# Performance work log

Hardware: AMD Instinct MI355X
Metric: run time of the kernel (lower is better)

The kernel has to match this reference:

```python
import jax, jax.numpy as jnp
import numpy as np

B, IN_SEQ, HID_SEQ, OUT_SEQ = 2, 2048, 2048, 2048
C_IN, C_OUT, H = 1024, 1024, 16
HD = C_OUT // H  # 64


def _linear_params(key, out_f, in_f):
    kw, kb = jax.random.split(key)
    bound = 1.0 / np.sqrt(in_f)
    w = jax.random.uniform(kw, (out_f, in_f), jnp.float32, -bound, bound)
    b = jax.random.uniform(kb, (out_f,), jnp.float32, -bound, bound)
    return w, b


def setup_inputs() -> dict:
    key = jax.random.key(0)
    ks = jax.random.split(key, 6)
    x = jax.random.normal(ks[0], (B, IN_SEQ, C_IN), jnp.float32)
    w_hseq, b_hseq = _linear_params(ks[1], HID_SEQ, IN_SEQ)
    wq, bq = _linear_params(ks[2], C_OUT, C_IN)
    wk, bk = _linear_params(ks[3], C_OUT, C_IN)
    wv, bv = _linear_params(ks[4], C_OUT, C_IN)
    w_oseq, b_oseq = _linear_params(ks[5], OUT_SEQ, HID_SEQ)
    return {"x": x, "w_hseq": w_hseq, "b_hseq": b_hseq,
            "wq": wq, "bq": bq, "wk": wk, "bk": bk, "wv": wv, "bv": bv,
            "w_oseq": w_oseq, "b_oseq": b_oseq}


def reference(x, w_hseq, b_hseq, wq, bq, wk, bk, wv, bv, w_oseq, b_oseq):
    b = x.shape[0]
    # seq-axis projection: Linear(in_seq -> hidden_seq) applied to x.transpose(1,2)
    # xh[b, t, c] = sum_s x[b, s, c] * w_hseq[t, s] + b_hseq[t]
    xh = jnp.einsum('bsc,ts->btc', x, w_hseq) + b_hseq[:, None]
    q = (xh @ wq.T + bq).reshape(b, HID_SEQ, H, HD).transpose(0, 2, 1, 3)  # [B,H,Sh,hd]
    k = (xh @ wk.T + bk).reshape(b, HID_SEQ, H, HD).transpose(0, 2, 1, 3)
    v = (xh @ wv.T + bv).reshape(b, HID_SEQ, H, HD).transpose(0, 2, 1, 3)
    scores = jnp.einsum('bhqd,bhkd->bhqk', q, k) / np.sqrt(HD).astype(np.float32)
    attn = jax.nn.softmax(scores, axis=-1)                       # [B,H,Sh,Sh]
    flex = jnp.einsum('bhqk,ok->bhqo', attn, w_oseq) + b_oseq    # [B,H,Sh,So]
    # flexscale.transpose(-2,-1) @ v contracts over the QUERY axis q
    out = jnp.einsum('bhqo,bhqd->bhod', flex, v)                 # [B,H,So,hd]
    return out.transpose(0, 2, 1, 3).reshape(b, OUT_SEQ, C_OUT)
```

## Files before the change

### kernel.cpp

```cpp
#include <hip/hip_runtime.h>
#include <hip/hip_bf16.h>

typedef unsigned short u16;
typedef unsigned int u32;
typedef unsigned long long u64;
typedef __attribute__((ext_vector_type(8))) short s16x8;
typedef __attribute__((ext_vector_type(4))) float f32x4;
typedef __attribute__((ext_vector_type(16))) float f32x16;

#define SCL 0.1803368867f

#if __has_builtin(__builtin_amdgcn_exp2f)
#define EXP2(x) __builtin_amdgcn_exp2f(x)
#else
#define EXP2(x) exp2f(x)
#endif

__device__ __forceinline__ float bf2f(u16 v){ u32 u = ((u32)v)<<16; return __builtin_bit_cast(float,u); }
__device__ __forceinline__ u16 f2bf(float f){
  u32 u = __builtin_bit_cast(u32,f);
  u += 0x7fff + ((u>>16)&1);
  return (u16)(u>>16);
}
__device__ __forceinline__ u32 pkbf(float a, float b){
  u32 ua = __builtin_bit_cast(u32,a) + 0x8000u;
  u32 ub = __builtin_bit_cast(u32,b) + 0x8000u;
  return (ua>>16) | (ub & 0xFFFF0000u);
}
__device__ __forceinline__ void glds16(const u16* g, const u16* lds_u){
  __builtin_amdgcn_global_load_lds(
      (const __attribute__((address_space(1))) void*)(u64)g,
      (__attribute__((address_space(3))) void*)(u32)(u64)lds_u,
      16, 0, 0);
}
__device__ __forceinline__ f32x4 mfma16(s16x8 a, s16x8 b, f32x4 c){
  return __builtin_amdgcn_mfma_f32_16x16x32_bf16(a,b,c,0,0,0);
}
__device__ __forceinline__ f32x16 mfma32(s16x8 a, s16x8 b, f32x16 c){
  return __builtin_amdgcn_mfma_f32_32x32x16_bf16(a,b,c,0,0,0);
}

__global__ __launch_bounds__(256) void detect_dtype(const u16* __restrict__ x, u32* __restrict__ flag){
  __shared__ int cnt;
  if (threadIdx.x==0) cnt = 0;
  __syncthreads();
  int local = 0;
  for (int i = threadIdx.x; i < 4096; i += 256){
    u16 v = x[2*i];
    int e = (v>>7)&0xFF;
    if (e >= 140 || e <= 100) local++;
  }
  atomicAdd(&cnt, local);
  __syncthreads();
  if (threadIdx.x==0) *flag = (cnt > 1024) ? 1u : 0u;
}

struct CvtArgs { const void* src[10]; u16* dst[10]; int n[10]; };

__global__ __launch_bounds__(256) void convert_all(
    CvtArgs a, const void* __restrict__ xsrc,
    const u32* __restrict__ flag, u16* __restrict__ xT)
{
  __shared__ u16 T[64][72];
  const int t = threadIdx.x;
  if (blockIdx.y < 10){
    const int which = blockIdx.y;
    const int n = a.n[which];
    const int base = blockIdx.x*2048 + t;
    if (base >= n) return;
    u16* dst = a.dst[which];
    if (*flag){
      const float* s = (const float*)a.src[which];
      #pragma unroll
      for (int j=0;j<8;j++){ int i = base + j*256; if (i<n) dst[i] = f2bf(s[i]); }
    } else {
      const u16* s = (const u16*)a.src[which];
      #pragma unroll
      for (int j=0;j<8;j++){ int i = base + j*256; if (i<n) dst[i] = s[i]; }
    }
    return;
  }
  const int bx = blockIdx.x;
  if (bx >= 1024) return;
  const int s0 = (bx&31)*64, c0 = ((bx>>5)&15)*64, b = bx>>9;
  const int r = t>>2, cc = (t&3)*16;
  const long off = ((long)(b*2048 + s0 + r))*1024 + c0 + cc;
  if (*flag){
    const float* p = (const float*)xsrc + off;
    #pragma unroll
    for (int j=0;j<16;j++) T[r][cc+j] = f2bf(p[j]);
  } else {
    const u16* p = (const u16*)xsrc + off;
    *(s16x8*)&T[r][cc]   = *(const s16x8*)p;
    *(s16x8*)&T[r][cc+8] = *(const s16x8*)(p+8);
  }
  __syncthreads();
  {
    const int orow = t&63, oc = (t>>6)*16;
    u16 tmp[16];
    #pragma unroll
    for (int j=0;j<16;j++) tmp[j] = T[oc+j][orow];
    u16* q = xT + (long)b*2097152 + (long)(c0+orow)*2048 + s0 + oc;
    *(s16x8*)q     = *(s16x8*)&tmp[0];
    *(s16x8*)(q+8) = *(s16x8*)&tmp[8];
  }
}

__global__ __launch_bounds__(256) void rowsum_mt(const u16* __restrict__ Mt, float* __restrict__ sv){
  const int row = blockIdx.x*4 + (threadIdx.x>>6);
  const int lane = threadIdx.x&63;
  const u16* p = Mt + (long)row*2048;
  float s = 0.f;
  #pragma unroll
  for (int i=0;i<4;i++){
    s16x8 v = *(const s16x8*)&p[i*512 + lane*8];
    #pragma unroll
    for (int j=0;j<8;j++) s += bf2f((u16)v[j]);
  }
  #pragma unroll
  for (int off=32; off>=1; off>>=1) s += __shfl_xor(s, off);
  if (lane==0) sv[row] = s;
}

template<int BN, int BMODE, bool DYN, bool QS>
__global__ __launch_bounds__(256) void gemm_t(
    const u16* __restrict__ A, const u16* __restrict__ B,
    const u16* __restrict__ bias, const float* __restrict__ r1col,
    const u32* __restrict__ dflag, void* __restrict__ C,
    int K, int lda, int ldb, int ldc,
    long aBatch, long bBatch, long cBatch)
{
  constexpr int BM = 128;
  constexpr int ACH = BM/64, BCH = BN/64;
  constexpr int MI = (BN==128) ? 4 : 2;
  __shared__ u16 As[2][BM*32];
  __shared__ u16 Bs[2][BN*32];
  const int t = threadIdx.x, w = t>>6, quad = (t&63)>>4, l16 = t&15;
  const int z = blockIdx.z;
  const int m0 = blockIdx.x*BM, n0 = blockIdx.y*BN;
  const u16* Ag = A + (long)z*aBatch + (long)m0*lda;
  const u16* Bg = B + (long)z*bBatch + (long)n0*ldb;
  const int wm = (BN==128) ? (w>>1)*64 : w*32;
  const int wn = (BN==128) ? (w&1)*64 : 0;

  auto stage = [&](int buf, int k0){
    #pragma unroll
    for (int i=0;i<ACH;i++){
      const int chunk = i*256 + t;
      glds16(Ag + (long)(chunk>>2)*lda + k0 + (chunk&3)*8, &As[buf][(i*256 + w*64)*8]);
    }
    #pragma unroll
    for (int i=0;i<BCH;i++){
      const int chunk = i*256 + t;
      glds16(Bg + (long)(chunk>>2)*ldb + k0 + (chunk&3)*8, &Bs[buf][(i*256 + w*64)*8]);
    }
  };

  f32x4 acc[MI][4];
  #pragma unroll
  for (int i=0;i<MI;i++)
    #pragma unroll
    for (int j=0;j<4;j++) acc[i][j] = (f32x4){0.f,0.f,0.f,0.f};

  stage(0, 0);
  const int nk = K>>5;
  for (int kt=0; kt<nk; ++kt){
    __syncthreads();
    if (kt+1 < nk) stage((kt+1)&1, (kt+1)<<5);
    const u16* as = As[kt&1];
    const u16* bs = Bs[kt&1];
    s16x8 a[MI], bb[4];
    #pragma unroll
    for (int i=0;i<MI;i++) a[i] = *(const s16x8*)&as[(wm + i*16 + l16)*32 + quad*8];
    #pragma unroll
    for (int j=0;j<4;j++)  bb[j]= *(const s16x8*)&bs[(wn + j*16 + l16)*32 + quad*8];
    #pragma unroll
    for (int i=0;i<MI;i++)
      #pragma unroll
      for (int j=0;j<4;j++)
        acc[i][j] = mfma16(a[i], bb[j], acc[i][j]);
  }

  bool f32o = false;
  if (DYN) f32o = (*dflag != 0);
  #pragma unroll
  for (int i=0;i<MI;i++){
    #pragma unroll
    for (int j=0;j<4;j++){
      const int col = n0 + wn + j*16 + l16;
      #pragma unroll
      for (int r=0;r<4;r++){
        const int row = m0 + wm + i*16 + quad*4 + r;
        float vv = acc[i][j][r];
        if (BMODE==1) vv += bf2f(bias[row]);
        if (BMODE==2) vv += bf2f(bias[col]);
        if (BMODE==3) vv += bf2f(bias[row]) * r1col[z*1024 + col];
        if (QS){ if (col < 1024) vv *= SCL; }
        const long idx = (long)z*cBatch + (long)row*ldc + col;
        if (DYN && f32o) ((float*)C)[idx] = vv;
        else             ((u16*)C)[idx]   = f2bf(vv);
      }
    }
  }
}

__global__ __launch_bounds__(256) void attn_stats(const u16* __restrict__ qkv, u16* __restrict__ VtG){
  __shared__ u16 Qs[64][68];
  __shared__ u16 Ks[64][68];
  __shared__ float red[2][64];
  __shared__ float ilv[64];
  const int q0 = blockIdx.x*64, bh = blockIdx.y, b = bh>>4, h = bh&15;
  const int t = threadIdx.x, w = t>>6, l32 = t&31, half = (t&63)>>5;
  const int wq = w>>1, wk = w&1;
  const int r = t>>2, cc = (t&3)*16;
  {
    const u16* p = &qkv[((long)(b*2048 + q0 + r))*3072 + h*64 + cc];
    *(s16x8*)&Qs[r][cc]   = *(const s16x8*)p;
    *(s16x8*)&Qs[r][cc+8] = *(const s16x8*)(p+8);
  }
  const u16* kg = &qkv[((long)(b*2048 + r))*3072 + 1024 + h*64 + cc];
  s16x8 sk0 = *(const s16x8*)kg;
  s16x8 sk1 = *(const s16x8*)(kg+8);
  __syncthreads();
  s16x8 aq[4];
  #pragma unroll
  for (int u=0;u<4;u++) aq[u] = *(s16x8*)&Qs[wq*32 + l32][u*16 + half*8];
  float lp[16];
  #pragma unroll
  for (int r2=0;r2<16;r2++) lp[r2] = 0.f;

  for (int kc=0; kc<2048; kc+=64){
    __syncthreads();
    *(s16x8*)&Ks[r][cc]   = sk0;
    *(s16x8*)&Ks[r][cc+8] = sk1;
    __syncthreads();
    if (kc+64 < 2048){
      const u16* nk = kg + (long)(kc+64)*3072;
      sk0 = *(const s16x8*)nk;
      sk1 = *(const s16x8*)(nk+8);
    }
    s16x8 kb[4];
    #pragma unroll
    for (int u=0;u<4;u++) kb[u] = *(s16x8*)&Ks[wk*32 + l32][u*16 + half*8];
    f32x16 acc = {};
    #pragma unroll
    for (int u=0;u<4;u++) acc = mfma32(aq[u], kb[u], acc);
    #pragma unroll
    for (int r2=0;r2<16;r2++) lp[r2] += EXP2(acc[r2]);
  }
  #pragma unroll
  for (int off=1; off<32; off<<=1)
    #pragma unroll
    for (int r2=0;r2<16;r2++) lp[r2] += __shfl_xor(lp[r2], off);
  if (l32 == 0){
    #pragma unroll
    for (int r2=0;r2<16;r2++)
      red[wk][wq*32 + 4*half + (r2&3) + 8*(r2>>2)] = lp[r2];
  }
  __syncthreads();
  if (t < 64) ilv[t] = 1.f / (red[0][t] + red[1][t]);
  __syncthreads();
  {
    const u16* p = &qkv[((long)(b*2048 + q0 + r))*3072 + 2048 + h*64 + cc];
    const float sc = ilv[r];
    s16x8 v0 = *(const s16x8*)p, v1 = *(const s16x8*)(p+8);
    #pragma unroll
    for (int j=0;j<8;j++){
      Qs[r][cc+j]   = f2bf(bf2f((u16)v0[j])*sc);
      Qs[r][cc+8+j] = f2bf(bf2f((u16)v1[j])*sc);
    }
  }
  __syncthreads();
  {
    const int orow = t&63, oc = (t>>6)*16;
    u16 tmp[16];
    #pragma unroll
    for (int j=0;j<16;j++) tmp[j] = Qs[oc+j][orow];
    u16* q = VtG + (long)b*2097152 + (long)(h*64+orow)*2048 + q0 + oc;
    *(s16x8*)q     = *(s16x8*)&tmp[0];
    *(s16x8*)(q+8) = *(s16x8*)&tmp[8];
  }
}

__global__ __launch_bounds__(256) void attn_pv(
    const u16* __restrict__ qkv, const u16* __restrict__ VtG, u16* __restrict__ Mt)
{
  __shared__ u16 Ks[64][68];
  __shared__ u16 Qs[64][68];
  __shared__ u16 Vs[64][68];
  __shared__ u16 Ps[64][68];
  const int k0 = blockIdx.x*64, bh = blockIdx.y, b = bh>>4, h = bh&15;
  const int t = threadIdx.x, w = t>>6, l32 = t&31, half = (t&63)>>5;
  const int wr = w>>1, wk = w&1;
  const int r = t>>2, cc = (t&3)*16;
  {
    const u16* p = &qkv[((long)(b*2048 + k0 + r))*3072 + 1024 + h*64 + cc];
    *(s16x8*)&Ks[r][cc]   = *(const s16x8*)p;
    *(s16x8*)&Ks[r][cc+8] = *(const s16x8*)(p+8);
  }
  const u16* qg = &qkv[((long)(b*2048 + r))*3072 + h*64 + cc];
  const u16* vg = &VtG[((long)(b*1024 + h*64 + r))*2048 + cc];
  s16x8 sq0 = *(const s16x8*)qg, sq1 = *(const s16x8*)(qg+8);
  s16x8 sv0 = *(const s16x8*)vg, sv1 = *(const s16x8*)(vg+8);
  __syncthreads();
  s16x8 kb[4];
  #pragma unroll
  for (int u=0;u<4;u++) kb[u] = *(s16x8*)&Ks[wk*32 + l32][u*16 + half*8];

  f32x16 accM = {};
  for (int q0=0; q0<2048; q0+=64){
    __syncthreads();
    *(s16x8*)&Qs[r][cc]   = sq0;
    *(s16x8*)&Qs[r][cc+8] = sq1;
    *(s16x8*)&Vs[r][cc]   = sv0;
    *(s16x8*)&Vs[r][cc+8] = sv1;
    __syncthreads();
    if (q0+64 < 2048){
      const u16* nq = qg + (long)(q0+64)*3072;
      const u16* nv = vg + (q0+64);
      sq0 = *(const s16x8*)nq; sq1 = *(const s16x8*)(nq+8);
      sv0 = *(const s16x8*)nv; sv1 = *(const s16x8*)(nv+8);
    }
    s16x8 aq[4];
    #pragma unroll
    for (int u=0;u<4;u++) aq[u] = *(s16x8*)&Qs[wr*32 + l32][u*16 + half*8];
    f32x16 acc = {};
    #pragma unroll
    for (int u=0;u<4;u++) acc = mfma32(aq[u], kb[u], acc);
    const int kcol = wk*32 + l32;
    #pragma unroll
    for (int g=0; g<4; g++){
      float p0 = EXP2(acc[4*g+0]);
      float p1 = EXP2(acc[4*g+1]);
      float p2 = EXP2(acc[4*g+2]);
      float p3 = EXP2(acc[4*g+3]);
      u64 v = (u64)pkbf(p0,p1) | ((u64)pkbf(p2,p3) << 32);
      *(u64*)&Ps[kcol][wr*32 + 8*g + 4*half] = v;
    }
    __syncthreads();
    s16x8 av[4], bp[4];
    #pragma unroll
    for (int u=0;u<4;u++) av[u] = *(s16x8*)&Vs[wr*32 + l32][u*16 + half*8];
    #pragma unroll
    for (int u=0;u<4;u++) bp[u] = *(s16x8*)&Ps[wk*32 + l32][u*16 + half*8];
    #pragma unroll
    for (int u=0;u<4;u++) accM = mfma32(av[u], bp[u], accM);
  }
  #pragma unroll
  for (int r2=0;r2<16;r2++){
    const int d = wr*32 + 4*half + (r2&3) + 8*(r2>>2);
    const int k = k0 + wk*32 + l32;
    Mt[((long)(b*1024 + h*64 + d))*2048 + k] = f2bf(accM[r2]);
  }
}

extern "C" void kernel_launch(void* const* d_in, const int* in_sizes, int n_in,
                              void* d_out, int out_size, void* d_ws, size_t ws_size,
                              hipStream_t stream)
{
  (void)n_in; (void)out_size; (void)ws_size;
  char* ws = (char*)d_ws;
  u32*  dflag = (u32*)ws;            ws += 64;
  u16*  whc   = (u16*)ws;            ws += (size_t)8388608;
  u16*  wqkvc = (u16*)ws;            ws += (size_t)6291456;
  u16*  woc   = (u16*)ws;            ws += (size_t)8388608;
  u16*  bhc   = (u16*)ws;            ws += 4096;
  u16*  bqkvc = (u16*)ws;            ws += 8192;
  u16*  boc   = (u16*)ws;            ws += 4096;
  u16*  xT    = (u16*)ws;            ws += (size_t)8388608;
  u16*  xh    = (u16*)ws;            ws += (size_t)8388608;
  u16*  qkvb  = (u16*)ws;            ws += (size_t)25165824;
  u16*  VtG   = (u16*)ws;            ws += (size_t)8388608;
  u16*  Mt    = (u16*)ws;            ws += (size_t)8388608;
  float* sv   = (float*)ws;          ws += 8192;

  detect_dtype<<<1,256,0,stream>>>((const u16*)d_in[0], dflag);
  CvtArgs ca;
  const void* srcs[10] = {d_in[1], d_in[2], d_in[3], d_in[4], d_in[5],
                          d_in[6], d_in[7], d_in[8], d_in[9], d_in[10]};
  u16* dsts[10] = {whc, bhc, wqkvc, bqkvc, wqkvc+1048576, bqkvc+1024,
                   wqkvc+2097152, bqkvc+2048, woc, boc};
  const int ns[10] = {in_sizes[1], in_sizes[2], in_sizes[3], in_sizes[4], in_sizes[5],
                      in_sizes[6], in_sizes[7], in_sizes[8], in_sizes[9], in_sizes[10]};
  for (int i=0;i<10;i++){ ca.src[i]=srcs[i]; ca.dst[i]=dsts[i]; ca.n[i]=ns[i]; }
  convert_all<<<dim3(2048,11),256,0,stream>>>(ca, d_in[0], dflag, xT);

  const long S2M = 2097152L;

  gemm_t<64,1,false,false><<<dim3(16,16,2),256,0,stream>>>(whc, xT, bhc, nullptr, dflag, xh,
      2048, 2048, 2048, 1024, 0L, S2M, S2M);

  gemm_t<128,2,false,true><<<dim3(16,24,2),256,0,stream>>>(xh, wqkvc, bqkvc, nullptr, dflag, qkvb,
      1024, 1024, 1024, 3072, S2M, 0L, (long)2048*3072);

  attn_stats<<<dim3(32,32),256,0,stream>>>(qkvb, VtG);

  attn_pv<<<dim3(32,32),256,0,stream>>>(qkvb, VtG, Mt);

  rowsum_mt<<<512,256,0,stream>>>(Mt, sv);

  gemm_t<64,3,true,false><<<dim3(16,16,2),256,0,stream>>>(woc, Mt, boc, sv, dflag, d_out,
      2048, 2048, 2048, 1024, 0L, S2M, S2M);
}
```

Baseline: 323.8 us.

## Rewrite attn_pv to keep P in registers via permlane swaps, drop LDS

The attention P·V kernel no longer stages Q, K, V and P through shared memory. Each wave now owns 32 key columns and loads its operands straight from global memory into registers. The exponentiated scores are repacked into the MFMA B-operand layout with v_permlane32_swap instead of an LDS transpose, which removes every __syncthreads in the loop. Each block now covers 128 keys, so the grid is halved and launch bounds ask for 2 blocks per SM. The cost is more redundant global/L2 traffic for Q and V across waves and higher register pressure.

```diff
diff --git a/kernel.cpp b/kernel.cpp
--- a/kernel.cpp
+++ b/kernel.cpp
@@ -5,6 +5,7 @@
 typedef unsigned int u32;
 typedef unsigned long long u64;
 typedef __attribute__((ext_vector_type(8))) short s16x8;
+typedef __attribute__((ext_vector_type(4))) u32 u32x4;
 typedef __attribute__((ext_vector_type(4))) float f32x4;
 typedef __attribute__((ext_vector_type(16))) float f32x16;
 
@@ -282,75 +283,77 @@
   }
 }
 
-__global__ __launch_bounds__(256) void attn_pv(
+__global__ __launch_bounds__(256,2) void attn_pv(
     const u16* __restrict__ qkv, const u16* __restrict__ VtG, u16* __restrict__ Mt)
 {
-  __shared__ u16 Ks[64][68];
-  __shared__ u16 Qs[64][68];
-  __shared__ u16 Vs[64][68];
-  __shared__ u16 Ps[64][68];
-  const int k0 = blockIdx.x*64, bh = blockIdx.y, b = bh>>4, h = bh&15;
-  const int t = threadIdx.x, w = t>>6, l32 = t&31, half = (t&63)>>5;
-  const int wr = w>>1, wk = w&1;
-  const int r = t>>2, cc = (t&3)*16;
-  {
-    const u16* p = &qkv[((long)(b*2048 + k0 + r))*3072 + 1024 + h*64 + cc];
-    *(s16x8*)&Ks[r][cc]   = *(const s16x8*)p;
-    *(s16x8*)&Ks[r][cc+8] = *(const s16x8*)(p+8);
-  }
-  const u16* qg = &qkv[((long)(b*2048 + r))*3072 + h*64 + cc];
-  const u16* vg = &VtG[((long)(b*1024 + h*64 + r))*2048 + cc];
-  s16x8 sq0 = *(const s16x8*)qg, sq1 = *(const s16x8*)(qg+8);
-  s16x8 sv0 = *(const s16x8*)vg, sv1 = *(const s16x8*)(vg+8);
-  __syncthreads();
+  const int t = threadIdx.x, w = t>>6, l32 = t&31, hi = (t&63)>>5;
+  const int bh = blockIdx.y, b = bh>>4, h = bh&15;
+  const int kcol = blockIdx.x*128 + w*32 + l32;
+  const u16* kp = qkv + ((long)(b*2048 + kcol))*3072 + 1024 + h*64 + hi*8;
+  const u16* qp = qkv + ((long)(b*2048 + l32))*3072 + h*64 + hi*8;
+  const u16* vp = VtG + ((long)(b*1024 + h*64 + l32))*2048 + hi*8;
+
   s16x8 kb[4];
   #pragma unroll
-  for (int u=0;u<4;u++) kb[u] = *(s16x8*)&Ks[wk*32 + l32][u*16 + half*8];
-
-  f32x16 accM = {};
+  for (int c=0;c<4;c++) kb[c] = *(const s16x8*)(kp + c*16);
+
+  s16x8 aqp[2][4];
+  #pragma unroll
+  for (int qt=0;qt<2;qt++)
+    #pragma unroll
+    for (int c=0;c<4;c++)
+      aqp[qt][c] = *(const s16x8*)(qp + (long)(qt*32)*3072 + c*16);
+
+  f32x16 accM0 = {}, accM1 = {};
   for (int q0=0; q0<2048; q0+=64){
-    __syncthreads();
-    *(s16x8*)&Qs[r][cc]   = sq0;
-    *(s16x8*)&Qs[r][cc+8] = sq1;
-    *(s16x8*)&Vs[r][cc]   = sv0;
-    *(s16x8*)&Vs[r][cc+8] = sv1;
-    __syncthreads();
+    s16x8 av[2][4];
+    #pragma unroll
+    for (int i=0;i<2;i++)
+      #pragma unroll
+      for (int c=0;c<4;c++)
+        av[i][c] = *(const s16x8*)(vp + (long)i*65536 + q0 + c*16);
+    f32x16 acc0 = {}, acc1 = {};
+    #pragma unroll
+    for (int c=0;c<4;c++){
+      acc0 = mfma32(aqp[0][c], kb[c], acc0);
+      acc1 = mfma32(aqp[1][c], kb[c], acc1);
+    }
     if (q0+64 < 2048){
-      const u16* nq = qg + (long)(q0+64)*3072;
-      const u16* nv = vg + (q0+64);
-      sq0 = *(const s16x8*)nq; sq1 = *(const s16x8*)(nq+8);
-      sv0 = *(const s16x8*)nv; sv1 = *(const s16x8*)(nv+8);
-    }
-    s16x8 aq[4];
-    #pragma unroll
-    for (int u=0;u<4;u++) aq[u] = *(s16x8*)&Qs[wr*32 + l32][u*16 + half*8];
-    f32x16 acc = {};
-    #pragma unroll
-    for (int u=0;u<4;u++) acc = mfma32(aq[u], kb[u], acc);
-    const int kcol = wk*32 + l32;
-    #pragma unroll
-    for (int g=0; g<4; g++){
-      float p0 = EXP2(acc[4*g+0]);
-      float p1 = EXP2(acc[4*g+1]);
-      float p2 = EXP2(acc[4*g+2]);
-      float p3 = EXP2(acc[4*g+3]);
-      u64 v = (u64)pkbf(p0,p1) | ((u64)pkbf(p2,p3) << 32);
-      *(u64*)&Ps[kcol][wr*32 + 8*g + 4*half] = v;
-    }
-    __syncthreads();
-    s16x8 av[4], bp[4];
-    #pragma unroll
-    for (int u=0;u<4;u++) av[u] = *(s16x8*)&Vs[wr*32 + l32][u*16 + half*8];
-    #pragma unroll
-    for (int u=0;u<4;u++) bp[u] = *(s16x8*)&Ps[wk*32 + l32][u*16 + half*8];
-    #pragma unroll
-    for (int u=0;u<4;u++) accM = mfma32(av[u], bp[u], accM);
+      #pragma unroll
+      for (int qt=0;qt<2;qt++)
+        #pragma unroll
+        for (int c=0;c<4;c++)
+          aqp[qt][c] = *(const s16x8*)(qp + (long)(q0+64+qt*32)*3072 + c*16);
+    }
+    s16x8 bp[4];
+    #pragma unroll
+    for (int qt=0;qt<2;qt++){
+      float p[16];
+      #pragma unroll
+      for (int r2=0;r2<16;r2++) p[r2] = EXP2(qt ? acc1[r2] : acc0[r2]);
+      #pragma unroll
+      for (int cc=0; cc<2; cc++){
+        u32 X0 = pkbf(p[cc*8+0], p[cc*8+1]);
+        u32 X1 = pkbf(p[cc*8+2], p[cc*8+3]);
+        u32 Y0 = pkbf(p[cc*8+4], p[cc*8+5]);
+        u32 Y1 = pkbf(p[cc*8+6], p[cc*8+7]);
+        asm volatile("v_permlane32_swap_b32 %0, %1" : "+v"(X0), "+v"(Y0));
+        asm volatile("v_permlane32_swap_b32 %0, %1" : "+v"(X1), "+v"(Y1));
+        u32x4 dw; dw[0]=X0; dw[1]=X1; dw[2]=Y0; dw[3]=Y1;
+        bp[qt*2+cc] = __builtin_bit_cast(s16x8, dw);
+      }
+    }
+    #pragma unroll
+    for (int c=0;c<4;c++){
+      accM0 = mfma32(av[0][c], bp[c], accM0);
+      accM1 = mfma32(av[1][c], bp[c], accM1);
+    }
   }
   #pragma unroll
   for (int r2=0;r2<16;r2++){
-    const int d = wr*32 + 4*half + (r2&3) + 8*(r2>>2);
-    const int k = k0 + wk*32 + l32;
-    Mt[((long)(b*1024 + h*64 + d))*2048 + k] = f2bf(accM[r2]);
+    const int d0 = 4*hi + (r2&3) + 8*(r2>>2);
+    Mt[((long)(b*1024 + h*64 + d0))*2048 + kcol]      = f2bf(accM0[r2]);
+    Mt[((long)(b*1024 + h*64 + d0 + 32))*2048 + kcol] = f2bf(accM1[r2]);
   }
 }
 
@@ -395,7 +398,7 @@
 
   attn_stats<<<dim3(32,32),256,0,stream>>>(qkvb, VtG);
 
-  attn_pv<<<dim3(32,32),256,0,stream>>>(qkvb, VtG, Mt);
+  attn_pv<<<dim3(16,32),256,0,stream>>>(qkvb, VtG, Mt);
 
   rowsum_mt<<<512,256,0,stream>>>(Mt, sv);
 
```

After: 370.3 us. 14.4% more time.
